# Performance work log

Hardware: AMD Instinct MI355X
Metric: run time of the kernel (lower is better)

The kernel has to match this reference:

```python
import jax, jax.numpy as jnp
import numpy as np

E = 8        # num_experts (material buckets)
L1 = 3072    # input dim
L2 = 15
L3 = 32
RF = 32      # ROUTER_FEATURES_PER_PERSPECTIVE
B = 16384
AUX_ALPHA = 0.01
Z_ALPHA = 0.001
LOAD_FLOOR = 0.05
LOAD_CAP = 0.5
PROBE_ALPHA = 0.01
PROBE_TAU = 1.0
PROBE_THRESH = 0.05
TEACHER_ALPHA = 0.0   # initial value of _teacher_alpha buffer
SCORE_SCALE = 600.0
SQ_SCALE = 255.0 / 256.0


def setup_inputs() -> dict:
    key = jax.random.key(0)
    ks = jax.random.split(key, 12)
    x = jax.random.uniform(ks[0], (B, L1), dtype=jnp.float32)
    ls_indices = jax.random.randint(ks[1], (B,), 0, E)
    psqt = jax.random.normal(ks[2], (B,), dtype=jnp.float32)
    score_target = jax.random.normal(ks[3], (B,), dtype=jnp.float32)
    router_w = 0.1 * jax.random.normal(ks[4], (E, 2 * RF), dtype=jnp.float32)
    router_b = jnp.zeros((E,), dtype=jnp.float32)
    # effective (coalesced) expert params, per _expert_params view
    w1 = jax.random.normal(ks[5], (E, L2 + 1, L1), dtype=jnp.float32) / np.sqrt(L1)
    b1 = 0.01 * jax.random.normal(ks[6], (E, L2 + 1), dtype=jnp.float32)
    w2 = jax.random.normal(ks[7], (E, L3, 2 * L2), dtype=jnp.float32) / np.sqrt(2 * L2)
    b2 = 0.01 * jax.random.normal(ks[8], (E, L3), dtype=jnp.float32)
    w3 = jax.random.normal(ks[9], (E, 1, L3), dtype=jnp.float32) / np.sqrt(L3)
    b3 = jnp.zeros((E, 1), dtype=jnp.float32)  # output bias zeroed in __init__
    return {"x": x, "ls_indices": ls_indices, "psqt": psqt,
            "score_target": score_target, "router_w": router_w,
            "router_b": router_b, "w1": w1, "b1": b1, "w2": w2, "b2": b2,
            "w3": w3, "b3": b3}


def _forward(x, psqt, score_target, router_w, router_b, w1, b1, w2, b2, w3, b3, ls_indices):
    half = L1 // 2
    router_in = jnp.concatenate([x[:, :RF], x[:, half:half + RF]], axis=1)  # [B, 64]
    gate_logits = router_in @ router_w.T + router_b                          # [B, E]
    logp = jax.nn.log_softmax(gate_logits, axis=-1)
    gate_probs = jnp.exp(logp)
    expert_indices = jnp.argmax(gate_logits, axis=-1)                        # [B]

    teacher_ce = -jnp.mean(jnp.take_along_axis(logp, ls_indices[:, None], axis=1))
    frac = jnp.bincount(expert_indices, length=E).astype(gate_probs.dtype) / gate_probs.shape[0]
    avg_gate = gate_probs.mean(axis=0)
    load = avg_gate + jax.lax.stop_gradient(frac - avg_gate)
    floor_loss = jnp.mean(jnp.square(jnp.maximum(LOAD_FLOOR - load, 0.0)))
    cap_loss = jnp.mean(jnp.square(jnp.maximum(load - LOAD_CAP, 0.0)))
    aux_loss = floor_loss + cap_loss
    z_loss = jnp.mean(jnp.square(jax.nn.logsumexp(gate_logits, axis=-1)))

    # ---- all-experts stacked MLP (fusion target) ----
    l1c = jnp.einsum('bi,eoi->beo', x, w1) + b1          # [B, E, L2+1]
    a, a_skip = l1c[..., :L2], l1c[..., L2:]              # [B,E,L2], [B,E,1]
    h = jnp.clip(jnp.concatenate([a * a * SQ_SCALE, a], axis=-1), 0.0, 1.0)  # [B,E,2*L2]
    l2x = jnp.clip(jnp.einsum('bei,eoi->beo', h, w2) + b2, 0.0, 1.0)         # [B,E,L3]
    all_out = jnp.einsum('bei,eoi->beo', l2x, w3) + b3 + a_skip              # [B,E,1]

    # ---- probe loss ----
    probe_weight = PROBE_ALPHA * max(PROBE_THRESH - TEACHER_ALPHA, 0.0) / max(PROBE_THRESH, 1e-9)
    expert_out = (all_out[..., 0] + psqt[:, None]) * SCORE_SCALE             # [B, E]
    err = jnp.square(expert_out - score_target[:, None])
    err = err - err.min(axis=1, keepdims=True)
    pt = jax.nn.softmax(-jax.lax.stop_gradient(err) / PROBE_TAU, axis=-1)
    log_pt = jnp.log(jnp.maximum(pt, 1e-30))
    probe_loss = jnp.mean(jnp.sum(pt * (log_pt - logp), axis=-1))            # kl_div batchmean

    router_loss = (AUX_ALPHA * aux_loss + Z_ALPHA * z_loss
                   + TEACHER_ALPHA * teacher_ce + probe_weight * probe_loss)

    l3x = jnp.take_along_axis(all_out, expert_indices[:, None, None], axis=1)[:, 0, :]  # [B, 1]
    gp = jnp.take_along_axis(gate_probs, expert_indices[:, None], axis=1)               # [B, 1]
    l3x = l3x * (1.0 + gp - jax.lax.stop_gradient(gp))  # straight-through (training mode)
    return l3x, router_loss


def reference(x, ls_indices, psqt, score_target, router_w, router_b, w1, b1, w2, b2, w3, b3):
    return _forward(x, psqt, score_target, router_w, router_b, w1, b1, w2, b2, w3, b3, ls_indices)
```

## Files before the change

kernel.cpp:

```cpp
#include <hip/hip_runtime.h>
#include <math.h>

#define BATCH 16384
#define K_DIM 3072
#define NOUT  128
#define NEXP  8

typedef float  f32x4  __attribute__((ext_vector_type(4)));
typedef __bf16 bf16x8 __attribute__((ext_vector_type(8)));
typedef unsigned int u32x4 __attribute__((ext_vector_type(4)));
typedef unsigned int u32x2 __attribute__((ext_vector_type(2)));

__device__ __forceinline__ unsigned short f2bf(float f) {
  union { float f; unsigned u; } v; v.f = f;
  unsigned u = v.u + 0x7fffu + ((v.u >> 16) & 1u);
  return (unsigned short)(u >> 16);
}

__device__ __forceinline__ bf16x8 asbf(u32x4 v) {
  union { u32x4 u; bf16x8 b; } c; c.u = v; return c.b;
}

__device__ __forceinline__ bf16x8 cvt8(f32x4 lo, f32x4 hi) {
  bf16x8 r;
  r[0] = (__bf16)lo[0]; r[1] = (__bf16)lo[1]; r[2] = (__bf16)lo[2]; r[3] = (__bf16)lo[3];
  r[4] = (__bf16)hi[0]; r[5] = (__bf16)hi[1]; r[6] = (__bf16)hi[2]; r[7] = (__bf16)hi[3];
  return r;
}

__global__ void cvt_w1_kernel(const float* __restrict__ w1, unsigned short* __restrict__ o,
                              float* __restrict__ accs) {
  if (blockIdx.x == 0 && threadIdx.x < 16) accs[threadIdx.x] = 0.f;
  int i = blockIdx.x * 256 + threadIdx.x;
  f32x4 v = ((const f32x4*)w1)[i];
  u32x2 p = { (unsigned)f2bf(v.x) | ((unsigned)f2bf(v.y) << 16),
              (unsigned)f2bf(v.z) | ((unsigned)f2bf(v.w) << 16) };
  ((u32x2*)o)[i] = p;
}

__global__ __launch_bounds__(256, 2) void moe_main_kernel(
    const float* __restrict__ x, const unsigned short* __restrict__ w1bf,
    const float* __restrict__ b1, const float* __restrict__ w2,
    const float* __restrict__ b2, const float* __restrict__ w3,
    const float* __restrict__ b3, const float* __restrict__ psqt,
    const float* __restrict__ st, const float* __restrict__ rw,
    const float* __restrict__ rb, float* __restrict__ out,
    float* __restrict__ accs) {
  __shared__ __align__(16) float Cl[32 * 132];
  __shared__ __align__(16) float w2s[8 * 964];
  __shared__ float b1s[128], b2s[256], w3s[256], b3s[8];
  __shared__ float rws[8 * 65];
  __shared__ float wred[4], zred[4];
  __shared__ int   hist[8];

  const int tid = threadIdx.x;
  const int bm  = blockIdx.x;

  for (int i = tid; i < 7680; i += 256) {
    int e = i / 960; int r = i - e * 960; int o = r / 30; int ii = r - o * 30;
    w2s[e * 964 + ii * 32 + o] = w2[i];
  }
  for (int i = tid; i < 512; i += 256) rws[(i >> 6) * 65 + (i & 63)] = rw[i];
  if (tid < 128) b1s[tid] = b1[tid];
  b2s[tid] = b2[tid];
  w3s[tid] = w3[tid];
  if (tid < 8) { b3s[tid] = b3[tid]; hist[tid] = 0; }
  __syncthreads();

  const int lane = tid & 63, wv = tid >> 6;
  const int l16 = lane & 15, lq = lane >> 4;
  const int rt = wv & 1;
  const int cb = (wv >> 1) * 4;

  const float*          pA = x    + (size_t)(bm * 32 + rt * 16 + l16) * K_DIM + lq * 8;
  const unsigned short* pB = w1bf + (size_t)(cb * 16 + l16) * K_DIM + lq * 8;

  f32x4 aR[2][4];
  u32x4 bR[2][8];

#define LOADT(S, KT) do {                                        \
    const float* pa_ = pA + (KT) * 64;                           \
    aR[S][0] = *(const f32x4*)(pa_);                             \
    aR[S][1] = *(const f32x4*)(pa_ + 4);                         \
    aR[S][2] = *(const f32x4*)(pa_ + 32);                        \
    aR[S][3] = *(const f32x4*)(pa_ + 36);                        \
    const unsigned short* pb_ = pB + (KT) * 64;                  \
    bR[S][0] = *(const u32x4*)(pb_);                             \
    bR[S][1] = *(const u32x4*)(pb_ + 32);                        \
    bR[S][2] = *(const u32x4*)(pb_ + 16 * K_DIM);                \
    bR[S][3] = *(const u32x4*)(pb_ + 16 * K_DIM + 32);           \
    bR[S][4] = *(const u32x4*)(pb_ + 32 * K_DIM);                \
    bR[S][5] = *(const u32x4*)(pb_ + 32 * K_DIM + 32);           \
    bR[S][6] = *(const u32x4*)(pb_ + 48 * K_DIM);                \
    bR[S][7] = *(const u32x4*)(pb_ + 48 * K_DIM + 32);           \
  } while (0)

#define COMPUTE(S) do {                                                              \
    bf16x8 af0 = cvt8(aR[S][0], aR[S][1]);                                           \
    bf16x8 af1 = cvt8(aR[S][2], aR[S][3]);                                           \
    _Pragma("unroll")                                                                \
    for (int c = 0; c < 4; ++c)                                                      \
      acc[c] = __builtin_amdgcn_mfma_f32_16x16x32_bf16(af0, asbf(bR[S][c * 2 + 0]),  \
                                                       acc[c], 0, 0, 0);             \
    _Pragma("unroll")                                                                \
    for (int c = 0; c < 4; ++c)                                                      \
      acc[c] = __builtin_amdgcn_mfma_f32_16x16x32_bf16(af1, asbf(bR[S][c * 2 + 1]),  \
                                                       acc[c], 0, 0, 0);             \
  } while (0)

  LOADT(0, 0);

  const int bl = tid >> 3, e = tid & 7;
  const int bg = bm * 32 + bl;
  const float* xrow = x + (size_t)bg * K_DIM;
  double lr = (double)rb[e];
#pragma unroll
  for (int c = 0; c < 32; ++c)
    lr = fma((double)xrow[c], (double)rws[e * 65 + c], lr);
#pragma unroll
  for (int c = 0; c < 32; ++c)
    lr = fma((double)xrow[1536 + c], (double)rws[e * 65 + 32 + c], lr);

  double mx = lr; int mi = e;
#pragma unroll
  for (int m = 1; m < 8; m <<= 1) {
    double ov = __shfl_xor(mx, m);
    int    oi = __shfl_xor(mi, m);
    if (ov > mx || (ov == mx && oi < mi)) { mx = ov; mi = oi; }
  }
  double ssum = exp(lr - mx);
#pragma unroll
  for (int m = 1; m < 8; m <<= 1) ssum += __shfl_xor(ssum, m);
  const double lse = mx + log(ssum);
  const float  logp_self = (float)(lr - lse);
  const int    rowEidx   = mi;

  if (e == 0) atomicAdd(&hist[rowEidx], 1);
  float zc = (e == 0) ? (float)(lse * lse) : 0.f;
#pragma unroll
  for (int m = 1; m < 64; m <<= 1) zc += __shfl_xor(zc, m);
  if (lane == 0) zred[wv] = zc;

  f32x4 acc[4];
#pragma unroll
  for (int c = 0; c < 4; ++c) acc[c] = (f32x4){0.f, 0.f, 0.f, 0.f};

#pragma unroll 1
  for (int kt = 0; kt < 48; kt += 2) {
    LOADT(1, kt + 1);
    COMPUTE(0);
    if (kt + 2 < 48) LOADT(0, kt + 2);
    COMPUTE(1);
  }

#pragma unroll
  for (int c = 0; c < 4; ++c)
#pragma unroll
    for (int r = 0; r < 4; ++r)
      Cl[(rt * 16 + lq * 4 + r) * 132 + (cb + c) * 16 + l16] = acc[c][r];
  __syncthreads();

  float a[16];
#pragma unroll
  for (int j = 0; j < 16; ++j) a[j] = Cl[bl * 132 + e * 16 + j] + b1s[e * 16 + j];

  float h[30];
#pragma unroll
  for (int j = 0; j < 15; ++j) {
    float v = a[j];
    h[j]      = fminf(fmaxf(v * v * (255.0f / 256.0f), 0.f), 1.f);
    h[15 + j] = fminf(fmaxf(v, 0.f), 1.f);
  }

  float acc2[32];
#pragma unroll
  for (int o = 0; o < 32; ++o) acc2[o] = b2s[e * 32 + o];
  const f32x4* wrow = (const f32x4*)&w2s[e * 964];
#pragma unroll
  for (int i = 0; i < 30; ++i) {
    float hv = h[i];
#pragma unroll
    for (int o4 = 0; o4 < 8; ++o4) {
      f32x4 wq = wrow[i * 8 + o4];
      acc2[o4 * 4 + 0] += hv * wq.x;
      acc2[o4 * 4 + 1] += hv * wq.y;
      acc2[o4 * 4 + 2] += hv * wq.z;
      acc2[o4 * 4 + 3] += hv * wq.w;
    }
  }

  float outv = b3s[e] + a[15];
#pragma unroll
  for (int o = 0; o < 32; ++o) {
    float l2v = fminf(fmaxf(acc2[o], 0.f), 1.f);
    outv += l2v * w3s[e * 32 + o];
  }

  float eo  = (outv + psqt[bg]) * 600.0f;
  float dd  = eo - st[bg];
  float err = dd * dd;
  float mn = err;
  mn = fminf(mn, __shfl_xor(mn, 1));
  mn = fminf(mn, __shfl_xor(mn, 2));
  mn = fminf(mn, __shfl_xor(mn, 4));
  float wexp = expf(-(err - mn));
  float ss = wexp;
  ss += __shfl_xor(ss, 1); ss += __shfl_xor(ss, 2); ss += __shfl_xor(ss, 4);
  float pt  = wexp / ss;
  float lpt = logf(fmaxf(pt, 1e-30f));
  float term = pt * (lpt - logp_self);
  term += __shfl_xor(term, 1); term += __shfl_xor(term, 2); term += __shfl_xor(term, 4);
  float c1 = (e == 0) ? term : 0.f;
  c1 += __shfl_xor(c1, 8); c1 += __shfl_xor(c1, 16); c1 += __shfl_xor(c1, 32);
  if (lane == 0) wred[wv] = c1;

  if (e == rowEidx) out[bg] = outv;

  __syncthreads();
  if (tid == 0) {
    atomicAdd(&accs[8], zred[0] + zred[1] + zred[2] + zred[3]);
    atomicAdd(&accs[9], wred[0] + wred[1] + wred[2] + wred[3]);
  }
  if (tid < 8) atomicAdd(&accs[tid], (float)hist[tid]);
#undef LOADT
#undef COMPUTE
}

__global__ void finalize_kernel(const float* __restrict__ accs, float* __restrict__ out) {
  if (threadIdx.x == 0) {
    float fsum = 0.f;
    for (int e = 0; e < 8; ++e) {
      float frac = accs[e] * (1.0f / 16384.0f);
      float f = fmaxf(0.05f - frac, 0.f);
      float c = fmaxf(frac - 0.5f, 0.f);
      fsum += f * f + c * c;
    }
    float aux   = fsum * 0.125f;
    float z     = accs[8] * (1.0f / 16384.0f);
    float probe = accs[9] * (1.0f / 16384.0f);
    out[BATCH] = 0.01f * aux + 0.001f * z + 0.01f * probe;
  }
}

extern "C" void kernel_launch(void* const* d_in, const int* in_sizes, int n_in,
                              void* d_out, int out_size, void* d_ws, size_t ws_size,
                              hipStream_t stream) {
  const float* x    = (const float*)d_in[0];
  const float* psqt = (const float*)d_in[2];
  const float* st   = (const float*)d_in[3];
  const float* rw   = (const float*)d_in[4];
  const float* rb   = (const float*)d_in[5];
  const float* w1   = (const float*)d_in[6];
  const float* b1   = (const float*)d_in[7];
  const float* w2   = (const float*)d_in[8];
  const float* b2   = (const float*)d_in[9];
  const float* w3   = (const float*)d_in[10];
  const float* b3   = (const float*)d_in[11];
  float* out = (float*)d_out;

  unsigned short* w1bf = (unsigned short*)d_ws;
  float* accs = (float*)((char*)d_ws + 786432);

  cvt_w1_kernel<<<384, 256, 0, stream>>>(w1, w1bf, accs);
  moe_main_kernel<<<512, 256, 0, stream>>>(x, w1bf, b1, w2, b2, w3, b3,
                                           psqt, st, rw, rb, out, accs);
  finalize_kernel<<<1, 1, 0, stream>>>(accs, out);
}
```

Measured before the change: 387.9 us.

## Stage GEMM tiles through LDS with direct global-to-LDS loads and swizzle

The main GEMM loop now copies x and bf16 w1 tiles into double-buffered shared memory with global_load_lds, using an XOR swizzle, and synchronises with explicit waitcnt and barriers. Before, each wave loaded its own operands into registers. The aim is to share tiles across waves, cut redundant global traffic and register pressure, and overlap loads with MFMA work. Small bias and router weight tables are now read directly from global memory instead of being copied into LDS. The larger LDS footprint (about 80KB) may limit occupancy, and the per-step barriers add synchronisation cost.

```diff
diff --git a/kernel.cpp b/kernel.cpp
--- a/kernel.cpp
+++ b/kernel.cpp
@@ -3,22 +3,15 @@
 
 #define BATCH 16384
 #define K_DIM 3072
-#define NOUT  128
-#define NEXP  8
 
 typedef float  f32x4  __attribute__((ext_vector_type(4)));
 typedef __bf16 bf16x8 __attribute__((ext_vector_type(8)));
-typedef unsigned int u32x4 __attribute__((ext_vector_type(4)));
 typedef unsigned int u32x2 __attribute__((ext_vector_type(2)));
 
 __device__ __forceinline__ unsigned short f2bf(float f) {
   union { float f; unsigned u; } v; v.f = f;
   unsigned u = v.u + 0x7fffu + ((v.u >> 16) & 1u);
   return (unsigned short)(u >> 16);
-}
-
-__device__ __forceinline__ bf16x8 asbf(u32x4 v) {
-  union { u32x4 u; bf16x8 b; } c; c.u = v; return c.b;
 }
 
 __device__ __forceinline__ bf16x8 cvt8(f32x4 lo, f32x4 hi) {
@@ -26,6 +19,12 @@
   r[0] = (__bf16)lo[0]; r[1] = (__bf16)lo[1]; r[2] = (__bf16)lo[2]; r[3] = (__bf16)lo[3];
   r[4] = (__bf16)hi[0]; r[5] = (__bf16)hi[1]; r[6] = (__bf16)hi[2]; r[7] = (__bf16)hi[3];
   return r;
+}
+
+__device__ __forceinline__ void gld16(const void* g, void* l) {
+  __builtin_amdgcn_global_load_lds(
+      (const __attribute__((address_space(1))) unsigned int*)g,
+      (__attribute__((address_space(3))) unsigned int*)l, 16, 0, 0);
 }
 
 __global__ void cvt_w1_kernel(const float* __restrict__ w1, unsigned short* __restrict__ o,
@@ -46,81 +45,101 @@
     const float* __restrict__ st, const float* __restrict__ rw,
     const float* __restrict__ rb, float* __restrict__ out,
     float* __restrict__ accs) {
-  __shared__ __align__(16) float Cl[32 * 132];
+  __shared__ __align__(16) unsigned char stage_sm[49152];
   __shared__ __align__(16) float w2s[8 * 964];
-  __shared__ float b1s[128], b2s[256], w3s[256], b3s[8];
-  __shared__ float rws[8 * 65];
-  __shared__ float wred[4], zred[4];
   __shared__ int   hist[8];
+  __shared__ float zred[4], wred[4];
 
   const int tid = threadIdx.x;
   const int bm  = blockIdx.x;
+  float* Cl = (float*)stage_sm;
 
   for (int i = tid; i < 7680; i += 256) {
     int e = i / 960; int r = i - e * 960; int o = r / 30; int ii = r - o * 30;
     w2s[e * 964 + ii * 32 + o] = w2[i];
   }
-  for (int i = tid; i < 512; i += 256) rws[(i >> 6) * 65 + (i & 63)] = rw[i];
-  if (tid < 128) b1s[tid] = b1[tid];
-  b2s[tid] = b2[tid];
-  w3s[tid] = w3[tid];
-  if (tid < 8) { b3s[tid] = b3[tid]; hist[tid] = 0; }
+  if (tid < 8) hist[tid] = 0;
   __syncthreads();
 
   const int lane = tid & 63, wv = tid >> 6;
   const int l16 = lane & 15, lq = lane >> 4;
   const int rt = wv & 1;
-  const int cb = (wv >> 1) * 4;
-
-  const float*          pA = x    + (size_t)(bm * 32 + rt * 16 + l16) * K_DIM + lq * 8;
-  const unsigned short* pB = w1bf + (size_t)(cb * 16 + l16) * K_DIM + lq * 8;
-
-  f32x4 aR[2][4];
-  u32x4 bR[2][8];
-
-#define LOADT(S, KT) do {                                        \
-    const float* pa_ = pA + (KT) * 64;                           \
-    aR[S][0] = *(const f32x4*)(pa_);                             \
-    aR[S][1] = *(const f32x4*)(pa_ + 4);                         \
-    aR[S][2] = *(const f32x4*)(pa_ + 32);                        \
-    aR[S][3] = *(const f32x4*)(pa_ + 36);                        \
-    const unsigned short* pb_ = pB + (KT) * 64;                  \
-    bR[S][0] = *(const u32x4*)(pb_);                             \
-    bR[S][1] = *(const u32x4*)(pb_ + 32);                        \
-    bR[S][2] = *(const u32x4*)(pb_ + 16 * K_DIM);                \
-    bR[S][3] = *(const u32x4*)(pb_ + 16 * K_DIM + 32);           \
-    bR[S][4] = *(const u32x4*)(pb_ + 32 * K_DIM);                \
-    bR[S][5] = *(const u32x4*)(pb_ + 32 * K_DIM + 32);           \
-    bR[S][6] = *(const u32x4*)(pb_ + 48 * K_DIM);                \
-    bR[S][7] = *(const u32x4*)(pb_ + 48 * K_DIM + 32);           \
+  const int cb = (wv >> 1) << 2;
+
+  const float* gA[2]; int lA[2];
+#pragma unroll
+  for (int r = 0; r < 2; ++r) {
+    int idx = r * 256 + tid; int row = idx >> 4; int blk = idx & 15;
+    gA[r] = x + (size_t)(bm * 32 + row) * K_DIM + ((blk ^ (row & 7)) << 2);
+    lA[r] = idx << 4;
+  }
+  const unsigned short* gB[4]; int lB[4];
+#pragma unroll
+  for (int r = 0; r < 4; ++r) {
+    int idx = r * 256 + tid; int row = idx >> 3; int blk = idx & 7;
+    gB[r] = w1bf + (size_t)row * K_DIM + ((blk ^ (row & 7)) << 3);
+    lB[r] = idx << 4;
+  }
+
+  const int arow = rt * 16 + l16;
+  int aoff[2], boff[2][4];
+#pragma unroll
+  for (int ks = 0; ks < 2; ++ks) {
+    aoff[ks] = arow * 256 + (((ks * 8 + lq * 2) ^ (arow & 7)) << 4);
+#pragma unroll
+    for (int cc = 0; cc < 4; ++cc) {
+      int o = (cb + cc) * 16 + l16;
+      boff[ks][cc] = o * 128 + (((lq + ks * 4) ^ (l16 & 7)) << 4);
+    }
+  }
+
+#define STAGE(C, KT) do {                                                  \
+    unsigned char* ab_ = stage_sm + (C) * 8192;                            \
+    unsigned char* bb_ = stage_sm + 16384 + (C) * 16384;                   \
+    gld16(gA[0] + (KT) * 64, ab_ + lA[0]);                                 \
+    gld16(gA[1] + (KT) * 64, ab_ + lA[1]);                                 \
+    gld16(gB[0] + (KT) * 64, bb_ + lB[0]);                                 \
+    gld16(gB[1] + (KT) * 64, bb_ + lB[1]);                                 \
+    gld16(gB[2] + (KT) * 64, bb_ + lB[2]);                                 \
+    gld16(gB[3] + (KT) * 64, bb_ + lB[3]);                                 \
   } while (0)
 
-#define COMPUTE(S) do {                                                              \
-    bf16x8 af0 = cvt8(aR[S][0], aR[S][1]);                                           \
-    bf16x8 af1 = cvt8(aR[S][2], aR[S][3]);                                           \
-    _Pragma("unroll")                                                                \
-    for (int c = 0; c < 4; ++c)                                                      \
-      acc[c] = __builtin_amdgcn_mfma_f32_16x16x32_bf16(af0, asbf(bR[S][c * 2 + 0]),  \
-                                                       acc[c], 0, 0, 0);             \
-    _Pragma("unroll")                                                                \
-    for (int c = 0; c < 4; ++c)                                                      \
-      acc[c] = __builtin_amdgcn_mfma_f32_16x16x32_bf16(af1, asbf(bR[S][c * 2 + 1]),  \
-                                                       acc[c], 0, 0, 0);             \
+#define COMPUTE(C) do {                                                    \
+    const unsigned char* ab_ = stage_sm + (C) * 8192;                      \
+    const unsigned char* bb_ = stage_sm + 16384 + (C) * 16384;             \
+    _Pragma("unroll")                                                      \
+    for (int ks = 0; ks < 2; ++ks) {                                       \
+      f32x4 a0 = *(const f32x4*)(ab_ + aoff[ks]);                          \
+      f32x4 a1 = *(const f32x4*)(ab_ + (aoff[ks] ^ 16));                   \
+      bf16x8 af = cvt8(a0, a1);                                            \
+      _Pragma("unroll")                                                    \
+      for (int cc = 0; cc < 4; ++cc) {                                     \
+        bf16x8 bfv = *(const bf16x8*)(bb_ + boff[ks][cc]);                 \
+        acc[cc] = __builtin_amdgcn_mfma_f32_16x16x32_bf16(af, bfv,         \
+                                                          acc[cc], 0,0,0); \
+      }                                                                    \
+    }                                                                      \
   } while (0)
-
-  LOADT(0, 0);
 
   const int bl = tid >> 3, e = tid & 7;
   const int bg = bm * 32 + bl;
-  const float* xrow = x + (size_t)bg * K_DIM;
+  const float* xrow  = x + (size_t)bg * K_DIM;
+  const float* rwrow = rw + e * 64;
   double lr = (double)rb[e];
 #pragma unroll
-  for (int c = 0; c < 32; ++c)
-    lr = fma((double)xrow[c], (double)rws[e * 65 + c], lr);
-#pragma unroll
-  for (int c = 0; c < 32; ++c)
-    lr = fma((double)xrow[1536 + c], (double)rws[e * 65 + 32 + c], lr);
-
+  for (int c4 = 0; c4 < 8; ++c4) {
+    f32x4 xv = *(const f32x4*)(xrow + c4 * 4);
+    f32x4 wvv = *(const f32x4*)(rwrow + c4 * 4);
+#pragma unroll
+    for (int j = 0; j < 4; ++j) lr = fma((double)xv[j], (double)wvv[j], lr);
+  }
+#pragma unroll
+  for (int c4 = 0; c4 < 8; ++c4) {
+    f32x4 xv = *(const f32x4*)(xrow + 1536 + c4 * 4);
+    f32x4 wvv = *(const f32x4*)(rwrow + 32 + c4 * 4);
+#pragma unroll
+    for (int j = 0; j < 4; ++j) lr = fma((double)xv[j], (double)wvv[j], lr);
+  }
   double mx = lr; int mi = e;
 #pragma unroll
   for (int m = 1; m < 8; m <<= 1) {
@@ -143,26 +162,48 @@
 
   f32x4 acc[4];
 #pragma unroll
-  for (int c = 0; c < 4; ++c) acc[c] = (f32x4){0.f, 0.f, 0.f, 0.f};
+  for (int cc = 0; cc < 4; ++cc) acc[cc] = (f32x4){0.f, 0.f, 0.f, 0.f};
+
+  asm volatile("s_waitcnt vmcnt(0)" ::: "memory");
+  STAGE(0, 0);
 
 #pragma unroll 1
-  for (int kt = 0; kt < 48; kt += 2) {
-    LOADT(1, kt + 1);
+  for (int kt = 0; kt < 46; kt += 2) {
+    STAGE(1, kt + 1);
+    asm volatile("s_waitcnt vmcnt(6)" ::: "memory");
+    __builtin_amdgcn_s_barrier();
     COMPUTE(0);
-    if (kt + 2 < 48) LOADT(0, kt + 2);
+    __builtin_amdgcn_s_barrier();
+    STAGE(0, kt + 2);
+    asm volatile("s_waitcnt vmcnt(6)" ::: "memory");
+    __builtin_amdgcn_s_barrier();
     COMPUTE(1);
-  }
-
-#pragma unroll
-  for (int c = 0; c < 4; ++c)
+    __builtin_amdgcn_s_barrier();
+  }
+  STAGE(1, 47);
+  asm volatile("s_waitcnt vmcnt(6)" ::: "memory");
+  __builtin_amdgcn_s_barrier();
+  COMPUTE(0);
+  __builtin_amdgcn_s_barrier();
+  asm volatile("s_waitcnt vmcnt(0)" ::: "memory");
+  __builtin_amdgcn_s_barrier();
+  COMPUTE(1);
+  __builtin_amdgcn_s_barrier();
+
+#pragma unroll
+  for (int cc = 0; cc < 4; ++cc)
 #pragma unroll
     for (int r = 0; r < 4; ++r)
-      Cl[(rt * 16 + lq * 4 + r) * 132 + (cb + c) * 16 + l16] = acc[c][r];
+      Cl[(rt * 16 + lq * 4 + r) * 132 + (cb + cc) * 16 + l16] = acc[cc][r];
   __syncthreads();
 
   float a[16];
-#pragma unroll
-  for (int j = 0; j < 16; ++j) a[j] = Cl[bl * 132 + e * 16 + j] + b1s[e * 16 + j];
+  {
+    const float* crow = Cl + bl * 132 + e * 16;
+    const float* b1p  = b1 + e * 16;
+#pragma unroll
+    for (int j = 0; j < 16; ++j) a[j] = crow[j] + b1p[j];
+  }
 
   float h[30];
 #pragma unroll
@@ -173,8 +214,15 @@
   }
 
   float acc2[32];
-#pragma unroll
-  for (int o = 0; o < 32; ++o) acc2[o] = b2s[e * 32 + o];
+  {
+    const f32x4* b2v = (const f32x4*)(b2 + e * 32);
+#pragma unroll
+    for (int o4 = 0; o4 < 8; ++o4) {
+      f32x4 t = b2v[o4];
+      acc2[o4 * 4 + 0] = t.x; acc2[o4 * 4 + 1] = t.y;
+      acc2[o4 * 4 + 2] = t.z; acc2[o4 * 4 + 3] = t.w;
+    }
+  }
   const f32x4* wrow = (const f32x4*)&w2s[e * 964];
 #pragma unroll
   for (int i = 0; i < 30; ++i) {
@@ -189,11 +237,17 @@
     }
   }
 
-  float outv = b3s[e] + a[15];
-#pragma unroll
-  for (int o = 0; o < 32; ++o) {
-    float l2v = fminf(fmaxf(acc2[o], 0.f), 1.f);
-    outv += l2v * w3s[e * 32 + o];
+  float outv = b3[e] + a[15];
+  {
+    const f32x4* w3v = (const f32x4*)(w3 + e * 32);
+#pragma unroll
+    for (int o4 = 0; o4 < 8; ++o4) {
+      f32x4 t = w3v[o4];
+      outv += fminf(fmaxf(acc2[o4 * 4 + 0], 0.f), 1.f) * t.x;
+      outv += fminf(fmaxf(acc2[o4 * 4 + 1], 0.f), 1.f) * t.y;
+      outv += fminf(fmaxf(acc2[o4 * 4 + 2], 0.f), 1.f) * t.z;
+      outv += fminf(fmaxf(acc2[o4 * 4 + 3], 0.f), 1.f) * t.w;
+    }
   }
 
   float eo  = (outv + psqt[bg]) * 600.0f;
@@ -222,7 +276,7 @@
     atomicAdd(&accs[9], wred[0] + wred[1] + wred[2] + wred[3]);
   }
   if (tid < 8) atomicAdd(&accs[tid], (float)hist[tid]);
-#undef LOADT
+#undef STAGE
 #undef COMPUTE
 }
 
```

New measurement: 333.2 us. -14.1%, faster.
